# Kernel optimization log

Measured on AMD Instinct MI355X. Metric: run time of the kernel, lower is better.

## Reference

```python
import jax, jax.numpy as jnp
import numpy as np

PROCESSING_SPEED = 8.0  # init kwarg: softmax temperature
EPS = 1e-8              # torch F.cosine_similarity eps
BATCH, SIZE, DIM = 1024, 65536, 512


def setup_inputs() -> dict:
    key = jax.random.key(0)
    k1, k2 = jax.random.split(key)
    x = jax.random.normal(k1, (BATCH, DIM), dtype=jnp.float32)
    memory_bank = jax.random.normal(k2, (SIZE, DIM), dtype=jnp.float32)
    return {"x": x, "memory_bank": memory_bank}


def reference(x, memory_bank):
    # Cosine similarity between every query and every memory row, computed as
    # normalized dot products (math-equivalent to F.cosine_similarity with
    # denominator clamp max(||a||*||b||, eps), avoiding the (B,S,D) broadcast).
    x_norm = jnp.linalg.norm(x, axis=1, keepdims=True)            # (B, 1)
    m_norm = jnp.linalg.norm(memory_bank, axis=1, keepdims=True)  # (S, 1)
    dots = jnp.einsum('bd,sd->bs', x, memory_bank)                # (B, S)
    sims = dots / jnp.maximum(x_norm * m_norm.T, EPS)             # (B, S)
    attention = jax.nn.softmax(sims * PROCESSING_SPEED, axis=1)   # (B, S)
    return attention @ memory_bank                                # (B, D)
```

## Files before the change

### kernel.cpp

```cpp
#include <hip/hip_runtime.h>
#include <hip/hip_bf16.h>
#include <stdint.h>

#define B_N 1024
#define S_N 65536
#define D_N 512
#define SCALE 8.0f
#define KSPLIT 16
#define KCHUNK (S_N / KSPLIT)

typedef __attribute__((ext_vector_type(8))) short bf16x8;
typedef __attribute__((ext_vector_type(4))) float f32x4;

#define OFF_MBF   ((size_t)0)
#define OFF_MT    (OFF_MBF + (size_t)S_N * D_N * 2)
#define OFF_XBF   (OFF_MT  + (size_t)D_N * S_N * 2)
#define OFF_P     (OFF_XBF + (size_t)B_N * D_N * 2)
#define OFF_XNSQ  (OFF_P   + (size_t)B_N * S_N * 2)
#define OFF_MNSQ  (OFF_XNSQ + (size_t)B_N * 4)
#define OFF_LSUM  (OFF_MNSQ + (size_t)S_N * 4)
#define OFF_OPART (OFF_LSUM + (size_t)B_N * 4)

__device__ __forceinline__ unsigned short f2bf(float f) {
  unsigned u = __builtin_bit_cast(unsigned, f);
  u += 0x7fffu + ((u >> 16) & 1u);
  return (unsigned short)(u >> 16);
}

__device__ __forceinline__ void stage16(const unsigned short* g, unsigned short* l) {
  __builtin_amdgcn_global_load_lds(
      (const __attribute__((address_space(1))) void*)g,
      (__attribute__((address_space(3))) void*)l, 16, 0, 0);
}

__global__ void k_prep_x(const float* __restrict__ X, unsigned short* __restrict__ Xbf,
                         float* __restrict__ xnsq) {
  const int row = blockIdx.x;
  const int t = threadIdx.x;
  float4 v = ((const float4*)(X + (size_t)row * D_N))[t];
  float ss = v.x*v.x + v.y*v.y + v.z*v.z + v.w*v.w;
  ushort4 o; o.x = f2bf(v.x); o.y = f2bf(v.y); o.z = f2bf(v.z); o.w = f2bf(v.w);
  ((ushort4*)(Xbf + (size_t)row * D_N))[t] = o;
  #pragma unroll
  for (int m = 1; m < 64; m <<= 1) ss += __shfl_xor(ss, m);
  __shared__ float partial[2];
  if ((t & 63) == 0) partial[t >> 6] = ss;
  __syncthreads();
  if (t == 0) xnsq[row] = partial[0] + partial[1];
}

__global__ void k_prep_m(const float* __restrict__ M, unsigned short* __restrict__ Mbf,
                         unsigned short* __restrict__ Mt, float* __restrict__ mnsq) {
  __shared__ float ts[64 * 65];
  const int t = threadIdx.x;
  const int s0 = blockIdx.x * 64;
  const int r = t >> 2, cq = t & 3;
  const int c = t >> 2, sq = t & 3;
  float ss = 0.f;
  for (int ct = 0; ct < 8; ++ct) {
    float f[16];
    const float4* src = (const float4*)(M + (size_t)(s0 + r) * D_N + ct * 64 + cq * 16);
    #pragma unroll
    for (int k = 0; k < 4; ++k) {
      float4 v = src[k];
      f[4*k+0] = v.x; f[4*k+1] = v.y; f[4*k+2] = v.z; f[4*k+3] = v.w;
    }
    union { unsigned short u[16]; uint4 v4[2]; } pk;
    #pragma unroll
    for (int j = 0; j < 16; ++j) {
      ss += f[j] * f[j];
      pk.u[j] = f2bf(f[j]);
      ts[r * 65 + cq * 16 + j] = f[j];
    }
    uint4* dst = (uint4*)(Mbf + (size_t)(s0 + r) * D_N + ct * 64 + cq * 16);
    dst[0] = pk.v4[0]; dst[1] = pk.v4[1];
    __syncthreads();
    union { unsigned short u[16]; uint4 v4[2]; } pt;
    #pragma unroll
    for (int j = 0; j < 16; ++j) pt.u[j] = f2bf(ts[(sq * 16 + j) * 65 + c]);
    uint4* dt = (uint4*)(Mt + (size_t)(ct * 64 + c) * S_N + s0 + sq * 16);
    dt[0] = pt.v4[0]; dt[1] = pt.v4[1];
    __syncthreads();
  }
  ss += __shfl_xor(ss, 1);
  ss += __shfl_xor(ss, 2);
  if (cq == 0) mnsq[s0 + r] = ss;
}

__global__ __launch_bounds__(256, 2) void k_qk(
    const unsigned short* __restrict__ Xbf, const unsigned short* __restrict__ Mbf,
    const float* __restrict__ xnsq, const float* __restrict__ mnsq,
    unsigned short* __restrict__ P, float* __restrict__ lsum) {
  __shared__ unsigned short As[128 * 64];
  __shared__ unsigned short Bs[128 * 64];
  const int t = threadIdx.x;
  const int w = t >> 6, lane = t & 63, quad = lane >> 4, l15 = lane & 15;
  const int wr = w >> 1, wc = w & 1;
  const int x7 = l15 & 7;
  const int bm = blockIdx.x, bn = blockIdx.y;

  f32x4 acc[4][4];
  #pragma unroll
  for (int i = 0; i < 4; ++i)
    #pragma unroll
    for (int j = 0; j < 4; ++j) acc[i][j] = (f32x4){0.f, 0.f, 0.f, 0.f};

  const int srow = t >> 3;
  const int schunk = (t & 7) ^ (srow & 7);
  const unsigned short* gA = Xbf + (size_t)(bm * 128 + srow) * D_N + schunk * 8;
  const unsigned short* gB = Mbf + (size_t)(bn * 128 + srow) * D_N + schunk * 8;
  unsigned short* lA = As + w * 512;
  unsigned short* lB = Bs + w * 512;

  for (int k0 = 0; k0 < D_N; k0 += 64) {
    #pragma unroll
    for (int i = 0; i < 4; ++i) {
      stage16(gA + (size_t)(i * 32) * D_N + k0, lA + i * 2048);
      stage16(gB + (size_t)(i * 32) * D_N + k0, lB + i * 2048);
    }
    __syncthreads();
    #pragma unroll
    for (int kk = 0; kk < 64; kk += 32) {
      const int cq = (kk >> 3) + quad;
      bf16x8 af[4], bfr[4];
      #pragma unroll
      for (int i = 0; i < 4; ++i)
        af[i] = *(const bf16x8*)&As[(wr * 64 + i * 16 + l15) * 64 + (cq ^ x7) * 8];
      #pragma unroll
      for (int j = 0; j < 4; ++j)
        bfr[j] = *(const bf16x8*)&Bs[(wc * 64 + j * 16 + l15) * 64 + (cq ^ x7) * 8];
      #pragma unroll
      for (int i = 0; i < 4; ++i)
        #pragma unroll
        for (int j = 0; j < 4; ++j)
          acc[i][j] = __builtin_amdgcn_mfma_f32_16x16x32_bf16(af[i], bfr[j], acc[i][j], 0, 0, 0);
    }
    __syncthreads();
  }

  float mn_[4];
  #pragma unroll
  for (int j = 0; j < 4; ++j) mn_[j] = mnsq[bn * 128 + wc * 64 + j * 16 + l15];
  #pragma unroll
  for (int i = 0; i < 4; ++i) {
    float rowsum[4];
    #pragma unroll
    for (int r = 0; r < 4; ++r) {
      const int b = bm * 128 + wr * 64 + i * 16 + quad * 4 + r;
      const float xq = xnsq[b];
      float rs = 0.f;
      #pragma unroll
      for (int j = 0; j < 4; ++j) {
        float d2 = fmaxf(xq * mn_[j], 1e-16f);
        float p = __expf(SCALE * acc[i][j][r] * rsqrtf(d2));
        rs += p;
        const int s = bn * 128 + wc * 64 + j * 16 + l15;
        P[(size_t)b * S_N + s] = f2bf(p);
      }
      rowsum[r] = rs;
    }
    #pragma unroll
    for (int r = 0; r < 4; ++r) {
      float rs = rowsum[r];
      rs += __shfl_xor(rs, 1);
      rs += __shfl_xor(rs, 2);
      rs += __shfl_xor(rs, 4);
      rs += __shfl_xor(rs, 8);
      if (l15 == 0) {
        const int b = bm * 128 + wr * 64 + i * 16 + quad * 4 + r;
        unsafeAtomicAdd(&lsum[b], rs);
      }
    }
  }
}

__global__ __launch_bounds__(256, 2) void k_pv(
    const unsigned short* __restrict__ P, const unsigned short* __restrict__ Mt,
    float* __restrict__ Opart) {
  __shared__ unsigned short As[128 * 64];
  __shared__ unsigned short Bs[128 * 64];
  const int t = threadIdx.x;
  const int w = t >> 6, lane = t & 63, quad = lane >> 4, l15 = lane & 15;
  const int wr = w >> 1, wc = w & 1;
  const int x7 = l15 & 7;
  const int bn = blockIdx.x, bm = blockIdx.y, ks = blockIdx.z;

  f32x4 acc[4][4];
  #pragma unroll
  for (int i = 0; i < 4; ++i)
    #pragma unroll
    for (int j = 0; j < 4; ++j) acc[i][j] = (f32x4){0.f, 0.f, 0.f, 0.f};

  const int srow = t >> 3;
  const int schunk = (t & 7) ^ (srow & 7);
  const unsigned short* gA = P  + (size_t)(bm * 128 + srow) * S_N + (size_t)ks * KCHUNK + schunk * 8;
  const unsigned short* gB = Mt + (size_t)(bn * 128 + srow) * S_N + (size_t)ks * KCHUNK + schunk * 8;
  unsigned short* lA = As + w * 512;
  unsigned short* lB = Bs + w * 512;

  for (int k0 = 0; k0 < KCHUNK; k0 += 64) {
    #pragma unroll
    for (int i = 0; i < 4; ++i) {
      stage16(gA + (size_t)(i * 32) * S_N + k0, lA + i * 2048);
      stage16(gB + (size_t)(i * 32) * S_N + k0, lB + i * 2048);
    }
    __syncthreads();
    #pragma unroll
    for (int kk = 0; kk < 64; kk += 32) {
      const int cq = (kk >> 3) + quad;
      bf16x8 af[4], bfr[4];
      #pragma unroll
      for (int i = 0; i < 4; ++i)
        af[i] = *(const bf16x8*)&As[(wr * 64 + i * 16 + l15) * 64 + (cq ^ x7) * 8];
      #pragma unroll
      for (int j = 0; j < 4; ++j)
        bfr[j] = *(const bf16x8*)&Bs[(wc * 64 + j * 16 + l15) * 64 + (cq ^ x7) * 8];
      #pragma unroll
      for (int i = 0; i < 4; ++i)
        #pragma unroll
        for (int j = 0; j < 4; ++j)
          acc[i][j] = __builtin_amdgcn_mfma_f32_16x16x32_bf16(af[i], bfr[j], acc[i][j], 0, 0, 0);
    }
    __syncthreads();
  }

  float* Od = Opart + (size_t)ks * (B_N * D_N);
  #pragma unroll
  for (int i = 0; i < 4; ++i)
    #pragma unroll
    for (int r = 0; r < 4; ++r) {
      const int b = bm * 128 + wr * 64 + i * 16 + quad * 4 + r;
      #pragma unroll
      for (int j = 0; j < 4; ++j) {
        const int d = bn * 128 + wc * 64 + j * 16 + l15;
        Od[(size_t)b * D_N + d] = acc[i][j][r];
      }
    }
}

__global__ void k_combine(const float* __restrict__ Opart, const float* __restrict__ lsum,
                          float* __restrict__ out) {
  const int idx = blockIdx.x * 256 + threadIdx.x;
  const int b = idx >> 7;
  float4 s = {0.f, 0.f, 0.f, 0.f};
  #pragma unroll
  for (int ks = 0; ks < KSPLIT; ++ks) {
    float4 v = ((const float4*)Opart)[(size_t)ks * (B_N * D_N / 4) + idx];
    s.x += v.x; s.y += v.y; s.z += v.z; s.w += v.w;
  }
  const float inv = 1.0f / lsum[b];
  s.x *= inv; s.y *= inv; s.z *= inv; s.w *= inv;
  ((float4*)out)[idx] = s;
}

extern "C" void kernel_launch(void* const* d_in, const int* in_sizes, int n_in,
                              void* d_out, int out_size, void* d_ws, size_t ws_size,
                              hipStream_t stream) {
  const float* X = (const float*)d_in[0];
  const float* M = (const float*)d_in[1];
  char* ws = (char*)d_ws;
  unsigned short* Mbf  = (unsigned short*)(ws + OFF_MBF);
  unsigned short* Mt   = (unsigned short*)(ws + OFF_MT);
  unsigned short* Xbf  = (unsigned short*)(ws + OFF_XBF);
  unsigned short* P    = (unsigned short*)(ws + OFF_P);
  float* xnsq = (float*)(ws + OFF_XNSQ);
  float* mnsq = (float*)(ws + OFF_MNSQ);
  float* lsum = (float*)(ws + OFF_LSUM);
  float* Opart = (float*)(ws + OFF_OPART);

  hipMemsetAsync(lsum, 0, B_N * sizeof(float), stream);
  k_prep_x<<<dim3(B_N), 128, 0, stream>>>(X, Xbf, xnsq);
  k_prep_m<<<dim3(S_N / 64), 256, 0, stream>>>(M, Mbf, Mt, mnsq);
  k_qk<<<dim3(8, S_N / 128), 256, 0, stream>>>(Xbf, Mbf, xnsq, mnsq, P, lsum);
  k_pv<<<dim3(D_N / 128, B_N / 128, KSPLIT), 256, 0, stream>>>(P, Mt, Opart);
  k_combine<<<dim3(B_N * D_N / 4 / 256), 256, 0, stream>>>(Opart, lsum, (float*)d_out);
}
```

Baseline: 488.4 us.

## Prefetch GEMM tiles through registers and use nontemporal stores for P and Mt

Both GEMM kernels stop using direct global-to-LDS loads. They now load the next K tile into registers while the current tile is computed, then write it into swizzled LDS, with a custom waitcnt-plus-barrier sync. The P writes in k_qk and the transposed Mt writes in k_prep_m become nontemporal stores to reduce cache pollution. Register prefetching can overlap global latency with MFMA work, but it raises register pressure and still uses one LDS buffer with two barriers per step.

```diff
diff --git a/kernel.cpp b/kernel.cpp
--- a/kernel.cpp
+++ b/kernel.cpp
@@ -11,6 +11,7 @@
 
 typedef __attribute__((ext_vector_type(8))) short bf16x8;
 typedef __attribute__((ext_vector_type(4))) float f32x4;
+typedef __attribute__((ext_vector_type(4))) unsigned int u32x4;
 
 #define OFF_MBF   ((size_t)0)
 #define OFF_MT    (OFF_MBF + (size_t)S_N * D_N * 2)
@@ -27,10 +28,16 @@
   return (unsigned short)(u >> 16);
 }
 
-__device__ __forceinline__ void stage16(const unsigned short* g, unsigned short* l) {
-  __builtin_amdgcn_global_load_lds(
-      (const __attribute__((address_space(1))) void*)g,
-      (__attribute__((address_space(3))) void*)l, 16, 0, 0);
+__device__ __forceinline__ void sync_lds_produce() {
+  asm volatile("" ::: "memory");
+  __builtin_amdgcn_s_waitcnt(0xC07F);
+  __builtin_amdgcn_s_barrier();
+  asm volatile("" ::: "memory");
+}
+__device__ __forceinline__ void sync_lds_consume() {
+  asm volatile("" ::: "memory");
+  __builtin_amdgcn_s_barrier();
+  asm volatile("" ::: "memory");
 }
 
 __global__ void k_prep_x(const float* __restrict__ X, unsigned short* __restrict__ Xbf,
@@ -75,11 +82,12 @@
     uint4* dst = (uint4*)(Mbf + (size_t)(s0 + r) * D_N + ct * 64 + cq * 16);
     dst[0] = pk.v4[0]; dst[1] = pk.v4[1];
     __syncthreads();
-    union { unsigned short u[16]; uint4 v4[2]; } pt;
+    union { unsigned short u[16]; u32x4 v4[2]; } pt;
     #pragma unroll
     for (int j = 0; j < 16; ++j) pt.u[j] = f2bf(ts[(sq * 16 + j) * 65 + c]);
-    uint4* dt = (uint4*)(Mt + (size_t)(ct * 64 + c) * S_N + s0 + sq * 16);
-    dt[0] = pt.v4[0]; dt[1] = pt.v4[1];
+    u32x4* dt = (u32x4*)(Mt + (size_t)(ct * 64 + c) * S_N + s0 + sq * 16);
+    __builtin_nontemporal_store(pt.v4[0], dt + 0);
+    __builtin_nontemporal_store(pt.v4[1], dt + 1);
     __syncthreads();
   }
   ss += __shfl_xor(ss, 1);
@@ -91,8 +99,8 @@
     const unsigned short* __restrict__ Xbf, const unsigned short* __restrict__ Mbf,
     const float* __restrict__ xnsq, const float* __restrict__ mnsq,
     unsigned short* __restrict__ P, float* __restrict__ lsum) {
-  __shared__ unsigned short As[128 * 64];
-  __shared__ unsigned short Bs[128 * 64];
+  __shared__ __align__(16) unsigned short As[128 * 64];
+  __shared__ __align__(16) unsigned short Bs[128 * 64];
   const int t = threadIdx.x;
   const int w = t >> 6, lane = t & 63, quad = lane >> 4, l15 = lane & 15;
   const int wr = w >> 1, wc = w & 1;
@@ -105,20 +113,34 @@
     #pragma unroll
     for (int j = 0; j < 4; ++j) acc[i][j] = (f32x4){0.f, 0.f, 0.f, 0.f};
 
-  const int srow = t >> 3;
-  const int schunk = (t & 7) ^ (srow & 7);
+  const int srow = t >> 3, schunk = t & 7;
+  const int sphys = schunk ^ (srow & 7);
   const unsigned short* gA = Xbf + (size_t)(bm * 128 + srow) * D_N + schunk * 8;
   const unsigned short* gB = Mbf + (size_t)(bn * 128 + srow) * D_N + schunk * 8;
-  unsigned short* lA = As + w * 512;
-  unsigned short* lB = Bs + w * 512;
-
-  for (int k0 = 0; k0 < D_N; k0 += 64) {
-    #pragma unroll
-    for (int i = 0; i < 4; ++i) {
-      stage16(gA + (size_t)(i * 32) * D_N + k0, lA + i * 2048);
-      stage16(gB + (size_t)(i * 32) * D_N + k0, lB + i * 2048);
-    }
-    __syncthreads();
+  uint4* wA = (uint4*)&As[srow * 64 + sphys * 8];
+  uint4* wB = (uint4*)&Bs[srow * 64 + sphys * 8];
+
+  uint4 rA[4], rB[4];
+  #pragma unroll
+  for (int i = 0; i < 4; ++i) {
+    rA[i] = *(const uint4*)(gA + (size_t)(i * 32) * D_N);
+    rB[i] = *(const uint4*)(gB + (size_t)(i * 32) * D_N);
+  }
+
+  #pragma unroll
+  for (int k0 = 0; k0 < 8; ++k0) {
+    #pragma unroll
+    for (int i = 0; i < 4; ++i) { wA[i * 256] = rA[i]; wB[i * 256] = rB[i]; }
+    if (k0 < 7) {
+      const unsigned short* nA = gA + (k0 + 1) * 64;
+      const unsigned short* nB = gB + (k0 + 1) * 64;
+      #pragma unroll
+      for (int i = 0; i < 4; ++i) {
+        rA[i] = *(const uint4*)(nA + (size_t)(i * 32) * D_N);
+        rB[i] = *(const uint4*)(nB + (size_t)(i * 32) * D_N);
+      }
+    }
+    sync_lds_produce();
     #pragma unroll
     for (int kk = 0; kk < 64; kk += 32) {
       const int cq = (kk >> 3) + quad;
@@ -135,7 +157,7 @@
         for (int j = 0; j < 4; ++j)
           acc[i][j] = __builtin_amdgcn_mfma_f32_16x16x32_bf16(af[i], bfr[j], acc[i][j], 0, 0, 0);
     }
-    __syncthreads();
+    sync_lds_consume();
   }
 
   float mn_[4];
@@ -155,7 +177,7 @@
         float p = __expf(SCALE * acc[i][j][r] * rsqrtf(d2));
         rs += p;
         const int s = bn * 128 + wc * 64 + j * 16 + l15;
-        P[(size_t)b * S_N + s] = f2bf(p);
+        __builtin_nontemporal_store(f2bf(p), &P[(size_t)b * S_N + s]);
       }
       rowsum[r] = rs;
     }
@@ -177,8 +199,8 @@
 __global__ __launch_bounds__(256, 2) void k_pv(
     const unsigned short* __restrict__ P, const unsigned short* __restrict__ Mt,
     float* __restrict__ Opart) {
-  __shared__ unsigned short As[128 * 64];
-  __shared__ unsigned short Bs[128 * 64];
+  __shared__ __align__(16) unsigned short As[128 * 64];
+  __shared__ __align__(16) unsigned short Bs[128 * 64];
   const int t = threadIdx.x;
   const int w = t >> 6, lane = t & 63, quad = lane >> 4, l15 = lane & 15;
   const int wr = w >> 1, wc = w & 1;
@@ -191,20 +213,33 @@
     #pragma unroll
     for (int j = 0; j < 4; ++j) acc[i][j] = (f32x4){0.f, 0.f, 0.f, 0.f};
 
-  const int srow = t >> 3;
-  const int schunk = (t & 7) ^ (srow & 7);
+  const int srow = t >> 3, schunk = t & 7;
+  const int sphys = schunk ^ (srow & 7);
   const unsigned short* gA = P  + (size_t)(bm * 128 + srow) * S_N + (size_t)ks * KCHUNK + schunk * 8;
   const unsigned short* gB = Mt + (size_t)(bn * 128 + srow) * S_N + (size_t)ks * KCHUNK + schunk * 8;
-  unsigned short* lA = As + w * 512;
-  unsigned short* lB = Bs + w * 512;
-
-  for (int k0 = 0; k0 < KCHUNK; k0 += 64) {
-    #pragma unroll
-    for (int i = 0; i < 4; ++i) {
-      stage16(gA + (size_t)(i * 32) * S_N + k0, lA + i * 2048);
-      stage16(gB + (size_t)(i * 32) * S_N + k0, lB + i * 2048);
-    }
-    __syncthreads();
+  uint4* wA = (uint4*)&As[srow * 64 + sphys * 8];
+  uint4* wB = (uint4*)&Bs[srow * 64 + sphys * 8];
+
+  uint4 rA[4], rB[4];
+  #pragma unroll
+  for (int i = 0; i < 4; ++i) {
+    rA[i] = *(const uint4*)(gA + (size_t)(i * 32) * S_N);
+    rB[i] = *(const uint4*)(gB + (size_t)(i * 32) * S_N);
+  }
+
+  for (int k0 = 0; k0 < KCHUNK / 64; ++k0) {
+    #pragma unroll
+    for (int i = 0; i < 4; ++i) { wA[i * 256] = rA[i]; wB[i * 256] = rB[i]; }
+    if (k0 < KCHUNK / 64 - 1) {
+      const unsigned short* nA = gA + (k0 + 1) * 64;
+      const unsigned short* nB = gB + (k0 + 1) * 64;
+      #pragma unroll
+      for (int i = 0; i < 4; ++i) {
+        rA[i] = *(const uint4*)(nA + (size_t)(i * 32) * S_N);
+        rB[i] = *(const uint4*)(nB + (size_t)(i * 32) * S_N);
+      }
+    }
+    sync_lds_produce();
     #pragma unroll
     for (int kk = 0; kk < 64; kk += 32) {
       const int cq = (kk >> 3) + quad;
@@ -221,7 +256,7 @@
         for (int j = 0; j < 4; ++j)
           acc[i][j] = __builtin_amdgcn_mfma_f32_16x16x32_bf16(af[i], bfr[j], acc[i][j], 0, 0, 0);
     }
-    __syncthreads();
+    sync_lds_consume();
   }
 
   float* Od = Opart + (size_t)ks * (B_N * D_N);
@@ -268,7 +303,7 @@
   float* lsum = (float*)(ws + OFF_LSUM);
   float* Opart = (float*)(ws + OFF_OPART);
 
-  hipMemsetAsync(lsum, 0, B_N * sizeof(float), stream);
+  (void)hipMemsetAsync(lsum, 0, B_N * sizeof(float), stream);
   k_prep_x<<<dim3(B_N), 128, 0, stream>>>(X, Xbf, xnsq);
   k_prep_m<<<dim3(S_N / 64), 256, 0, stream>>>(M, Mbf, Mt, mnsq);
   k_qk<<<dim3(8, S_N / 128), 256, 0, stream>>>(Xbf, Mbf, xnsq, mnsq, P, lsum);
```

After: 1.185 ms. +142.7%, slower.
